# Optimization experiments

Measured on AMD Instinct MI355X. Metric: run time of the kernel, lower is better.

The kernel has to match this reference:

```python
import jax, jax.numpy as jnp
import numpy as np

N, E = 50000, 800000
DIM_IN, DIM_H, DIM_OUT, HEADS = 128, 16, 64, 8
NEG_SLOPE = 0.2  # PyG GATv2Conv default


def setup_inputs() -> dict:
    key = jax.random.key(0)
    ks = jax.random.split(key, 10)
    s = 0.1
    x = jax.random.normal(ks[0], (N, DIM_IN), jnp.float32)
    edge_index = jax.random.randint(ks[1], (2, E), 0, N, dtype=jnp.int32)
    Wl1 = jax.random.normal(ks[2], (DIM_IN, HEADS * DIM_H), jnp.float32) * s
    Wr1 = jax.random.normal(ks[3], (DIM_IN, HEADS * DIM_H), jnp.float32) * s
    att1 = jax.random.normal(ks[4], (HEADS, DIM_H), jnp.float32) * s
    b1 = jnp.zeros((HEADS * DIM_H,), jnp.float32)
    Wl2 = jax.random.normal(ks[5], (HEADS * DIM_H, DIM_OUT), jnp.float32) * s
    Wr2 = jax.random.normal(ks[6], (HEADS * DIM_H, DIM_OUT), jnp.float32) * s
    att2 = jax.random.normal(ks[7], (1, DIM_OUT), jnp.float32) * s
    b2 = jnp.zeros((DIM_OUT,), jnp.float32)
    return dict(x=x, edge_index=edge_index, Wl1=Wl1, Wr1=Wr1, att1=att1, b1=b1,
                Wl2=Wl2, Wr2=Wr2, att2=att2, b2=b2)


def gatv2_conv(x, src, dst, Wl, Wr, att, bias, heads, out_ch):
    # PyG GATv2Conv (share_weights=False, concat=True)
    n = x.shape[0]
    xl = (x @ Wl).reshape(n, heads, out_ch)  # source-side transform
    xr = (x @ Wr).reshape(n, heads, out_ch)  # target-side transform
    e = jax.nn.leaky_relu(xl[src] + xr[dst], NEG_SLOPE)          # [E, H, C]
    logits = jnp.einsum('ehc,hc->eh', e, att)                    # [E, H]
    # segment softmax over incoming edges of each dst node
    m = jax.lax.stop_gradient(jax.ops.segment_max(logits, dst, num_segments=n))
    ex = jnp.exp(logits - m[dst])
    denom = jax.ops.segment_sum(ex, dst, num_segments=n)
    alpha = ex / denom[dst]                                      # [E, H]
    out = jax.ops.segment_sum(xl[src] * alpha[..., None], dst, num_segments=n)
    return out.reshape(n, heads * out_ch) + bias


def reference(x, edge_index, Wl1, Wr1, att1, b1, Wl2, Wr2, att2, b2):
    n = x.shape[0]
    loops = jnp.arange(n, dtype=edge_index.dtype)
    src = jnp.concatenate([edge_index[0], loops])  # add_self_loops=True
    dst = jnp.concatenate([edge_index[1], loops])
    h = gatv2_conv(x, src, dst, Wl1, Wr1, att1, b1, HEADS, DIM_H)
    h = jax.nn.elu(h)
    out = gatv2_conv(h, src, dst, Wl2, Wr2, att2, b2, 1, DIM_OUT)
    return jax.nn.log_softmax(out, axis=1)
```

## Files before the change

### kernel.cpp

```cpp
#include <hip/hip_runtime.h>
#include <cstdint>

#define DIM_IN 128
#define HEADS 8
#define DIM_H 16
#define H1 128
#define DIM_OUT 64
#define NEG 0.2f
#define CAP 6144

typedef __attribute__((ext_vector_type(8))) short bf16x8;
typedef __attribute__((ext_vector_type(4))) float f32x4;

__device__ __forceinline__ float blo(uint32_t u) { return __uint_as_float(u << 16); }
__device__ __forceinline__ float bhi(uint32_t u) { return __uint_as_float(u & 0xffff0000u); }
__device__ __forceinline__ unsigned short f2b(float f) {
  uint32_t u = __float_as_uint(f);
  u += 0x7fffu + ((u >> 16) & 1u);
  return (unsigned short)(u >> 16);
}

__global__ __launch_bounds__(256) void conv_x(
    const float* __restrict__ in, unsigned short* __restrict__ out, int total) {
  int i = (blockIdx.x * 256 + threadIdx.x) * 8;
  if (i >= total) return;
  float4 a = *(const float4*)(in + i);
  float4 b = *(const float4*)(in + i + 4);
  ushort4 u0 = {f2b(a.x), f2b(a.y), f2b(a.z), f2b(a.w)};
  ushort4 u1 = {f2b(b.x), f2b(b.y), f2b(b.z), f2b(b.w)};
  *(ushort4*)(out + i) = u0;
  *(ushort4*)(out + i + 4) = u1;
}

__global__ __launch_bounds__(256) void prep_w(
    const float* __restrict__ W0, const float* __restrict__ W1,
    const float* __restrict__ W2, const float* __restrict__ W3,
    unsigned short* __restrict__ T0, unsigned short* __restrict__ T1,
    unsigned short* __restrict__ T2, unsigned short* __restrict__ T3) {
  int z = blockIdx.y;
  const float* W = (z == 0) ? W0 : (z == 1) ? W1 : (z == 2) ? W2 : W3;
  unsigned short* T = (z == 0) ? T0 : (z == 1) ? T1 : (z == 2) ? T2 : T3;
  int M = (z < 2) ? 128 : 64;
  int t = blockIdx.x * 256 + threadIdx.x;
  if (t >= M * 128) return;
  int n = t >> 7, k = t & 127;
  T[t] = f2b(W[k * M + n]);
}

template <int M>
__global__ __launch_bounds__(256) void gemm_mfma(
    const unsigned short* __restrict__ A,
    const unsigned short* __restrict__ Bt0, const unsigned short* __restrict__ Bt1,
    unsigned short* __restrict__ Cb0, float* __restrict__ C1, int Nrows) {
  constexpr int K = 128;
  constexpr int LDA = 72;
  constexpr int MT = M / 2;
  constexpr int NT = MT / 16;
  __shared__ __align__(16) short Asm[128 * LDA];
  __shared__ __align__(16) short Bsm[M * LDA];
  const unsigned short* __restrict__ Bt = blockIdx.z ? Bt1 : Bt0;
  const int row0 = blockIdx.x * 128;
  const int tid = threadIdx.x;
  const int w = tid >> 6, lane = tid & 63;
  const int l = lane & 15, q = lane >> 4;
  const int wrow = (w >> 1) * 64, wcol = (w & 1) * MT;

  f32x4 zero = {0.f, 0.f, 0.f, 0.f};
  f32x4 acc[4][NT];
#pragma unroll
  for (int ti = 0; ti < 4; ++ti)
#pragma unroll
    for (int tj = 0; tj < NT; ++tj) acc[ti][tj] = zero;

  for (int k0 = 0; k0 < K; k0 += 64) {
    __syncthreads();
    {
      int r = tid >> 1, sg = (tid & 1) * 32;
      int grow = row0 + r;
      const uint4* src = (const uint4*)(A + (size_t)grow * K + k0 + sg);
      uint4 z4 = make_uint4(0, 0, 0, 0);
#pragma unroll
      for (int i = 0; i < 4; ++i) {
        uint4 v = (grow < Nrows) ? src[i] : z4;
        *(uint4*)(Asm + r * LDA + sg + i * 8) = v;
      }
    }
    {
      int r = tid >> 1, sg = (tid & 1) * 32;
      if (r < M) {
        const uint4* src = (const uint4*)(Bt + (size_t)r * K + k0 + sg);
#pragma unroll
        for (int i = 0; i < 4; ++i)
          *(uint4*)(Bsm + r * LDA + sg + i * 8) = src[i];
      }
    }
    __syncthreads();
#pragma unroll
    for (int kk = 0; kk < 64; kk += 32) {
      bf16x8 af[4], bfr[NT];
#pragma unroll
      for (int ti = 0; ti < 4; ++ti)
        af[ti] = *(const bf16x8*)(Asm + (wrow + ti * 16 + l) * LDA + kk + q * 8);
#pragma unroll
      for (int tj = 0; tj < NT; ++tj)
        bfr[tj] = *(const bf16x8*)(Bsm + (wcol + tj * 16 + l) * LDA + kk + q * 8);
#pragma unroll
      for (int ti = 0; ti < 4; ++ti)
#pragma unroll
        for (int tj = 0; tj < NT; ++tj)
          acc[ti][tj] = __builtin_amdgcn_mfma_f32_16x16x32_bf16(
              af[ti], bfr[tj], acc[ti][tj], 0, 0, 0);
    }
  }
#pragma unroll
  for (int ti = 0; ti < 4; ++ti) {
#pragma unroll
    for (int tj = 0; tj < NT; ++tj) {
      int col = wcol + tj * 16 + l;
#pragma unroll
      for (int r = 0; r < 4; ++r) {
        int grow = row0 + wrow + ti * 16 + q * 4 + r;
        if (grow < Nrows) {
          float vv = acc[ti][tj][r];
          if (blockIdx.z == 0) Cb0[(size_t)grow * M + col] = f2b(vv);
          else                 C1[(size_t)grow * M + col] = vv;
        }
      }
    }
  }
}

__global__ __launch_bounds__(256) void p1_bucket(
    const int* __restrict__ ei, int* __restrict__ gcnt,
    uint32_t* __restrict__ gbuf, int E, int nbkt) {
  __shared__ int hist[256];
  __shared__ int base[256];
  __shared__ int cur[256];
  int tid = threadIdx.x;
  hist[tid] = 0;
  __syncthreads();
  int e0 = blockIdx.x * 8192;
  int nE = min(8192, E - e0);
  for (int i = tid; i < nE; i += 256)
    atomicAdd(&hist[ei[E + e0 + i] >> 8], 1);
  __syncthreads();
  if (tid < nbkt) {
    int h = hist[tid];
    base[tid] = h ? atomicAdd(&gcnt[tid], h) : 0;
  }
  cur[tid] = 0;
  __syncthreads();
  for (int i = tid; i < nE; i += 256) {
    int d = ei[E + e0 + i];
    int s = ei[e0 + i];
    int b = d >> 8;
    int r = atomicAdd(&cur[b], 1);
    int pos = base[b] + r;
    if (pos < CAP) gbuf[(size_t)b * CAP + pos] = ((uint32_t)d << 16) | (uint32_t)s;
  }
}

__device__ __forceinline__ int block_excl_scan256(int v, int* tmp) {
  int lane = threadIdx.x & 63, wid = threadIdx.x >> 6;
  int x = v;
#pragma unroll
  for (int o = 1; o < 64; o <<= 1) {
    int y = __shfl_up(x, o, 64);
    if (lane >= o) x += y;
  }
  if (lane == 63) tmp[wid] = x;
  __syncthreads();
  int prefix = 0;
#pragma unroll
  for (int w = 0; w < 4; ++w) if (w < wid) prefix += tmp[w];
  __syncthreads();
  return prefix + x - v;
}

__global__ __launch_bounds__(256) void p2_fused(
    const uint32_t* __restrict__ gbuf, const int* __restrict__ gcnt,
    int* __restrict__ off, int* __restrict__ srcs, int N, int nbkt) {
  __shared__ int sb[256];
  __shared__ int hist[256];
  __shared__ int cur[256];
  __shared__ int tmp[4];
  int b = blockIdx.x, tid = threadIdx.x;
  int gv = (tid < nbkt) ? gcnt[tid] : 0;
  int gex = block_excl_scan256(gv, tmp);
  sb[tid] = gex;
  hist[tid] = 0;
  __syncthreads();
  int base = sb[b];
  int cnt = min(gcnt[b], CAP);
  const uint32_t* p = gbuf + (size_t)b * CAP;
  for (int i = tid; i < cnt; i += 256)
    atomicAdd(&hist[(p[i] >> 16) & 255], 1);
  __syncthreads();
  int d = hist[tid];
  int excl = block_excl_scan256(d, tmp);
  int idx = (b << 8) + tid;
  int o = base + excl;
  if (idx <= N) off[idx] = o;
  cur[tid] = o;
  __syncthreads();
  for (int i = tid; i < cnt; i += 256) {
    uint32_t v = p[i];
    int pos = atomicAdd(&cur[(v >> 16) & 255], 1);
    srcs[pos] = (int)(v & 0xFFFFu);
  }
}

__global__ __launch_bounds__(256) void agg_l1(
    const int* __restrict__ srcs, const int* __restrict__ off,
    const unsigned short* __restrict__ xlb, const float* __restrict__ xr,
    const float* __restrict__ att, const float* __restrict__ b1,
    unsigned short* __restrict__ hbb, int N) {
  int wid = threadIdx.x >> 6, lane = threadIdx.x & 63;
  int node = blockIdx.x * 4 + wid;
  if (node >= N) return;
  const int l4 = lane & 15;
  const int g  = lane >> 4;
  float4 xr0 = *(const float4*)(xr + ((size_t)node << 7) + (l4 << 3));
  float4 xr1 = *(const float4*)(xr + ((size_t)node << 7) + (l4 << 3) + 4);
  float4 a0  = *(const float4*)(att + (l4 << 3));
  float4 a1  = *(const float4*)(att + (l4 << 3) + 4);
  float acc0 = 0.f, acc1 = 0.f, acc2 = 0.f, acc3 = 0.f;
  float acc4 = 0.f, acc5 = 0.f, acc6 = 0.f, acc7 = 0.f;
  float dsum = 0.f;
  int beg = off[node];
  int M = off[node + 1] - beg + 1;
  for (int base = 0; base < M; base += 64) {
    int nk = min(64, M - base);
    int v = base + lane;
    int sv = 0;
    if (lane < nk) sv = (v == 0) ? node : srcs[beg + v - 1];
    int niter = (nk + 3) >> 2;
    for (int it = 0; it < niter; ++it) {
      int j = (it << 2) + g;
      int s = __shfl(sv, j, 64);
      uint4 xu = *(const uint4*)(xlb + ((size_t)s << 7) + (l4 << 3));
      float x0 = blo(xu.x), x1 = bhi(xu.x), x2 = blo(xu.y), x3 = bhi(xu.y);
      float x4 = blo(xu.z), x5 = bhi(xu.z), x6 = blo(xu.w), x7 = bhi(xu.w);
      float t, p;
      t = x0 + xr0.x; t = t > 0.f ? t : NEG * t; p = a0.x * t;
      t = x1 + xr0.y; t = t > 0.f ? t : NEG * t; p = fmaf(a0.y, t, p);
      t = x2 + xr0.z; t = t > 0.f ? t : NEG * t; p = fmaf(a0.z, t, p);
      t = x3 + xr0.w; t = t > 0.f ? t : NEG * t; p = fmaf(a0.w, t, p);
      t = x4 + xr1.x; t = t > 0.f ? t : NEG * t; p = fmaf(a1.x, t, p);
      t = x5 + xr1.y; t = t > 0.f ? t : NEG * t; p = fmaf(a1.y, t, p);
      t = x6 + xr1.z; t = t > 0.f ? t : NEG * t; p = fmaf(a1.z, t, p);
      t = x7 + xr1.w; t = t > 0.f ? t : NEG * t; p = fmaf(a1.w, t, p);
      p += __shfl_xor(p, 1, 64);
      float ev = (j < nk) ? __expf(p) : 0.f;
      acc0 = fmaf(ev, x0, acc0); acc1 = fmaf(ev, x1, acc1);
      acc2 = fmaf(ev, x2, acc2); acc3 = fmaf(ev, x3, acc3);
      acc4 = fmaf(ev, x4, acc4); acc5 = fmaf(ev, x5, acc5);
      acc6 = fmaf(ev, x6, acc6); acc7 = fmaf(ev, x7, acc7);
      dsum += ev;
    }
  }
#pragma unroll
  for (int o = 16; o <= 32; o <<= 1) {
    dsum += __shfl_xor(dsum, o, 64);
    acc0 += __shfl_xor(acc0, o, 64); acc1 += __shfl_xor(acc1, o, 64);
    acc2 += __shfl_xor(acc2, o, 64); acc3 += __shfl_xor(acc3, o, 64);
    acc4 += __shfl_xor(acc4, o, 64); acc5 += __shfl_xor(acc5, o, 64);
    acc6 += __shfl_xor(acc6, o, 64); acc7 += __shfl_xor(acc7, o, 64);
  }
  if (g == 0) {
    float inv = 1.0f / dsum;
    float4 bv0 = *(const float4*)(b1 + (l4 << 3));
    float4 bv1 = *(const float4*)(b1 + (l4 << 3) + 4);
    float o0 = fmaf(acc0, inv, bv0.x), o1 = fmaf(acc1, inv, bv0.y);
    float o2 = fmaf(acc2, inv, bv0.z), o3 = fmaf(acc3, inv, bv0.w);
    float o4 = fmaf(acc4, inv, bv1.x), o5 = fmaf(acc5, inv, bv1.y);
    float o6 = fmaf(acc6, inv, bv1.z), o7 = fmaf(acc7, inv, bv1.w);
    o0 = o0 > 0.f ? o0 : expm1f(o0); o1 = o1 > 0.f ? o1 : expm1f(o1);
    o2 = o2 > 0.f ? o2 : expm1f(o2); o3 = o3 > 0.f ? o3 : expm1f(o3);
    o4 = o4 > 0.f ? o4 : expm1f(o4); o5 = o5 > 0.f ? o5 : expm1f(o5);
    o6 = o6 > 0.f ? o6 : expm1f(o6); o7 = o7 > 0.f ? o7 : expm1f(o7);
    ushort4 h0 = {f2b(o0), f2b(o1), f2b(o2), f2b(o3)};
    ushort4 h1 = {f2b(o4), f2b(o5), f2b(o6), f2b(o7)};
    unsigned short* ph = hbb + ((size_t)node << 7) + (l4 << 3);
    *(ushort4*)(ph)     = h0;
    *(ushort4*)(ph + 4) = h1;
  }
}

__global__ __launch_bounds__(256) void agg_l2(
    const int* __restrict__ srcs, const int* __restrict__ off,
    const unsigned short* __restrict__ xlb, const float* __restrict__ xr,
    const float* __restrict__ att, const float* __restrict__ b2,
    float* __restrict__ out, int N) {
  int wid = threadIdx.x >> 6, lane = threadIdx.x & 63;
  int node = blockIdx.x * 4 + wid;
  if (node >= N) return;
  const int l3 = lane & 7;
  const int g  = lane >> 3;
  float4 xr0 = *(const float4*)(xr + ((size_t)node << 6) + (l3 << 3));
  float4 xr1 = *(const float4*)(xr + ((size_t)node << 6) + (l3 << 3) + 4);
  float4 a0  = *(const float4*)(att + (l3 << 3));
  float4 a1  = *(const float4*)(att + (l3 << 3) + 4);
  float acc0 = 0.f, acc1 = 0.f, acc2 = 0.f, acc3 = 0.f;
  float acc4 = 0.f, acc5 = 0.f, acc6 = 0.f, acc7 = 0.f;
  float dsum = 0.f;
  int beg = off[node];
  int M = off[node + 1] - beg + 1;
  for (int base = 0; base < M; base += 64) {
    int nk = min(64, M - base);
    int v = base + lane;
    int sv = 0;
    if (lane < nk) sv = (v == 0) ? node : srcs[beg + v - 1];
    int niter = (nk + 7) >> 3;
    for (int it = 0; it < niter; ++it) {
      int j = (it << 3) + g;
      int s = __shfl(sv, j, 64);
      uint4 xu = *(const uint4*)(xlb + ((size_t)s << 6) + (l3 << 3));
      float x0 = blo(xu.x), x1 = bhi(xu.x), x2 = blo(xu.y), x3 = bhi(xu.y);
      float x4 = blo(xu.z), x5 = bhi(xu.z), x6 = blo(xu.w), x7 = bhi(xu.w);
      float t, p;
      t = x0 + xr0.x; t = t > 0.f ? t : NEG * t; p = a0.x * t;
      t = x1 + xr0.y; t = t > 0.f ? t : NEG * t; p = fmaf(a0.y, t, p);
      t = x2 + xr0.z; t = t > 0.f ? t : NEG * t; p = fmaf(a0.z, t, p);
      t = x3 + xr0.w; t = t > 0.f ? t : NEG * t; p = fmaf(a0.w, t, p);
      t = x4 + xr1.x; t = t > 0.f ? t : NEG * t; p = fmaf(a1.x, t, p);
      t = x5 + xr1.y; t = t > 0.f ? t : NEG * t; p = fmaf(a1.y, t, p);
      t = x6 + xr1.z; t = t > 0.f ? t : NEG * t; p = fmaf(a1.z, t, p);
      t = x7 + xr1.w; t = t > 0.f ? t : NEG * t; p = fmaf(a1.w, t, p);
      p += __shfl_xor(p, 1, 64);
      p += __shfl_xor(p, 2, 64);
      p += __shfl_xor(p, 4, 64);
      float ev = (j < nk) ? __expf(p) : 0.f;
      acc0 = fmaf(ev, x0, acc0); acc1 = fmaf(ev, x1, acc1);
      acc2 = fmaf(ev, x2, acc2); acc3 = fmaf(ev, x3, acc3);
      acc4 = fmaf(ev, x4, acc4); acc5 = fmaf(ev, x5, acc5);
      acc6 = fmaf(ev, x6, acc6); acc7 = fmaf(ev, x7, acc7);
      dsum += ev;
    }
  }
#pragma unroll
  for (int o = 8; o <= 32; o <<= 1) {
    dsum += __shfl_xor(dsum, o, 64);
    acc0 += __shfl_xor(acc0, o, 64); acc1 += __shfl_xor(acc1, o, 64);
    acc2 += __shfl_xor(acc2, o, 64); acc3 += __shfl_xor(acc3, o, 64);
    acc4 += __shfl_xor(acc4, o, 64); acc5 += __shfl_xor(acc5, o, 64);
    acc6 += __shfl_xor(acc6, o, 64); acc7 += __shfl_xor(acc7, o, 64);
  }
  float inv = 1.0f / dsum;
  float4 bv0 = *(const float4*)(b2 + (l3 << 3));
  float4 bv1 = *(const float4*)(b2 + (l3 << 3) + 4);
  float v0 = fmaf(acc0, inv, bv0.x), v1 = fmaf(acc1, inv, bv0.y);
  float v2 = fmaf(acc2, inv, bv0.z), v3 = fmaf(acc3, inv, bv0.w);
  float v4 = fmaf(acc4, inv, bv1.x), v5 = fmaf(acc5, inv, bv1.y);
  float v6 = fmaf(acc6, inv, bv1.z), v7 = fmaf(acc7, inv, bv1.w);
  float m = fmaxf(fmaxf(fmaxf(v0, v1), fmaxf(v2, v3)),
                  fmaxf(fmaxf(v4, v5), fmaxf(v6, v7)));
#pragma unroll
  for (int o = 1; o <= 4; o <<= 1) m = fmaxf(m, __shfl_xor(m, o, 64));
  float s = __expf(v0 - m) + __expf(v1 - m) + __expf(v2 - m) + __expf(v3 - m)
          + __expf(v4 - m) + __expf(v5 - m) + __expf(v6 - m) + __expf(v7 - m);
#pragma unroll
  for (int o = 1; o <= 4; o <<= 1) s += __shfl_xor(s, o, 64);
  if (g == 0) {
    float ls = __logf(s) + m;
    float* po = out + ((size_t)node << 6) + (l3 << 3);
    *(float4*)(po)     = make_float4(v0 - ls, v1 - ls, v2 - ls, v3 - ls);
    *(float4*)(po + 4) = make_float4(v4 - ls, v5 - ls, v6 - ls, v7 - ls);
  }
}

extern "C" void kernel_launch(void* const* d_in, const int* in_sizes, int n_in,
                              void* d_out, int out_size, void* d_ws, size_t ws_size,
                              hipStream_t stream) {
  const float* x    = (const float*)d_in[0];
  const int*   ei   = (const int*)d_in[1];
  const float* Wl1  = (const float*)d_in[2];
  const float* Wr1  = (const float*)d_in[3];
  const float* att1 = (const float*)d_in[4];
  const float* b1   = (const float*)d_in[5];
  const float* Wl2  = (const float*)d_in[6];
  const float* Wr2  = (const float*)d_in[7];
  const float* att2 = (const float*)d_in[8];
  const float* b2   = (const float*)d_in[9];
  float* out = (float*)d_out;

  const int N = in_sizes[0] / DIM_IN;
  const int E = in_sizes[1] / 2;
  const int nb = (N + 255) / 256;

  float* ws = (float*)d_ws;
  const size_t szNH = (size_t)N * H1;
  float* xr1 = ws;
  float* xr2 = ws + szNH;
  unsigned short* xb   = (unsigned short*)(ws + szNH + (size_t)N * DIM_OUT);
  unsigned short* xlb1 = xb + szNH;
  unsigned short* hbb  = xlb1 + szNH;
  unsigned short* xlb2 = hbb + szNH;
  unsigned short* wt0  = xlb2 + (size_t)N * DIM_OUT;
  unsigned short* wt1  = wt0 + 16384;
  unsigned short* wt2  = wt1 + 16384;
  unsigned short* wt3  = wt2 + 8192;
  int* ibase  = (int*)(wt3 + 8192);
  int* off    = ibase;
  int* gcnt   = ibase + N + 1;
  int* srcs   = ibase + N + 1 + 256;
  uint32_t* gbuf = (uint32_t*)(srcs + E);

  hipMemsetAsync(gcnt, 0, 256 * sizeof(int), stream);
  p1_bucket<<<(E + 8191) / 8192, 256, 0, stream>>>(ei, gcnt, gbuf, E, nb);
  p2_fused<<<nb, 256, 0, stream>>>(gbuf, gcnt, off, srcs, N, nb);

  int totx = N * DIM_IN;
  conv_x<<<(totx / 8 + 255) / 256, 256, 0, stream>>>(x, xb, totx);
  prep_w<<<dim3(64, 4), 256, 0, stream>>>(Wl1, Wr1, Wl2, Wr2, wt0, wt1, wt2, wt3);

  const int gb = (N + 127) / 128;

  gemm_mfma<128><<<dim3(gb, 1, 2), 256, 0, stream>>>(xb, wt0, wt1, xlb1, xr1, N);
  agg_l1<<<(N + 3) / 4, 256, 0, stream>>>(srcs, off, xlb1, xr1, att1, b1, hbb, N);

  gemm_mfma<64><<<dim3(gb, 1, 2), 256, 0, stream>>>(hbb, wt2, wt3, xlb2, xr2, N);
  agg_l2<<<(N + 3) / 4, 256, 0, stream>>>(srcs, off, xlb2, xr2, att2, b2, out, N);
}
```

Before: 255.2 us.

## Split leaky-ReLU logits into per-node linear terms plus abs term, use exp2

Rewrites leaky_relu(z) as 0.6z + 0.4|z|, so the linear part of each attention logit splits into a per-source term (precomputed by new dotp kernels) and a per-destination term (computed once per node), and only the abs term stays in the per-edge loop. Constants are pre-scaled by log2(e) so exp2f replaces __expf. The x-conversion and weight-prep kernels are fused into one launch. In exchange it adds two small kernels, an extra per-edge scalar gather of dL, and slight rounding differences from the regrouped arithmetic.

```diff
diff --git a/kernel.cpp b/kernel.cpp
--- a/kernel.cpp
+++ b/kernel.cpp
@@ -8,6 +8,7 @@
 #define DIM_OUT 64
 #define NEG 0.2f
 #define CAP 6144
+#define L2E 1.4426950408889634f
 
 typedef __attribute__((ext_vector_type(8))) short bf16x8;
 typedef __attribute__((ext_vector_type(4))) float f32x4;
@@ -20,31 +21,71 @@
   return (unsigned short)(u >> 16);
 }
 
-__global__ __launch_bounds__(256) void conv_x(
-    const float* __restrict__ in, unsigned short* __restrict__ out, int total) {
-  int i = (blockIdx.x * 256 + threadIdx.x) * 8;
-  if (i >= total) return;
-  float4 a = *(const float4*)(in + i);
-  float4 b = *(const float4*)(in + i + 4);
-  ushort4 u0 = {f2b(a.x), f2b(a.y), f2b(a.z), f2b(a.w)};
-  ushort4 u1 = {f2b(b.x), f2b(b.y), f2b(b.z), f2b(b.w)};
-  *(ushort4*)(out + i) = u0;
-  *(ushort4*)(out + i + 4) = u1;
-}
-
-__global__ __launch_bounds__(256) void prep_w(
+__global__ __launch_bounds__(256) void prep_fused(
+    const float* __restrict__ x, unsigned short* __restrict__ xb, int totx,
     const float* __restrict__ W0, const float* __restrict__ W1,
     const float* __restrict__ W2, const float* __restrict__ W3,
     unsigned short* __restrict__ T0, unsigned short* __restrict__ T1,
-    unsigned short* __restrict__ T2, unsigned short* __restrict__ T3) {
-  int z = blockIdx.y;
-  const float* W = (z == 0) ? W0 : (z == 1) ? W1 : (z == 2) ? W2 : W3;
-  unsigned short* T = (z == 0) ? T0 : (z == 1) ? T1 : (z == 2) ? T2 : T3;
-  int M = (z < 2) ? 128 : 64;
+    unsigned short* __restrict__ T2, unsigned short* __restrict__ T3,
+    int xblocks) {
+  int bx = blockIdx.x;
+  if (bx < xblocks) {
+    int i = (bx * 256 + threadIdx.x) * 8;
+    if (i >= totx) return;
+    float4 a = *(const float4*)(x + i);
+    float4 b = *(const float4*)(x + i + 4);
+    ushort4 u0 = {f2b(a.x), f2b(a.y), f2b(a.z), f2b(a.w)};
+    ushort4 u1 = {f2b(b.x), f2b(b.y), f2b(b.z), f2b(b.w)};
+    *(ushort4*)(xb + i) = u0;
+    *(ushort4*)(xb + i + 4) = u1;
+  } else {
+    int wz = bx - xblocks;
+    int z = wz >> 6;
+    const float* W = (z == 0) ? W0 : (z == 1) ? W1 : (z == 2) ? W2 : W3;
+    unsigned short* T = (z == 0) ? T0 : (z == 1) ? T1 : (z == 2) ? T2 : T3;
+    int M = (z < 2) ? 128 : 64;
+    int t = (wz & 63) * 256 + threadIdx.x;
+    if (t >= M * 128) return;
+    int n = t >> 7, k = t & 127;
+    T[t] = f2b(W[k * M + n]);
+  }
+}
+
+__global__ __launch_bounds__(256) void dotp1(
+    const unsigned short* __restrict__ xlb, const float* __restrict__ att,
+    float* __restrict__ dL, int N8) {
   int t = blockIdx.x * 256 + threadIdx.x;
-  if (t >= M * 128) return;
-  int n = t >> 7, k = t & 127;
-  T[t] = f2b(W[k * M + n]);
+  if (t >= N8) return;
+  int h = t & 7;
+  const uint4* p = (const uint4*)(xlb + ((size_t)t << 4));
+  uint4 u0 = p[0], u1 = p[1];
+  const float4* pa = (const float4*)(att + (h << 4));
+  float4 a0 = pa[0], a1 = pa[1], a2 = pa[2], a3 = pa[3];
+  float s = a0.x * blo(u0.x) + a0.y * bhi(u0.x) + a0.z * blo(u0.y) + a0.w * bhi(u0.y)
+          + a1.x * blo(u0.z) + a1.y * bhi(u0.z) + a1.z * blo(u0.w) + a1.w * bhi(u0.w)
+          + a2.x * blo(u1.x) + a2.y * bhi(u1.x) + a2.z * blo(u1.y) + a2.w * bhi(u1.y)
+          + a3.x * blo(u1.z) + a3.y * bhi(u1.z) + a3.z * blo(u1.w) + a3.w * bhi(u1.w);
+  dL[t] = s * (0.6f * L2E);
+}
+
+__global__ __launch_bounds__(256) void dotp2(
+    const unsigned short* __restrict__ xlb, const float* __restrict__ att,
+    float* __restrict__ dL, int N) {
+  int t = blockIdx.x * 256 + threadIdx.x;
+  int n = t >> 1, half = t & 1;
+  if (n >= N) return;
+  const uint4* p = (const uint4*)(xlb + ((size_t)n << 6) + (half << 5));
+  const float4* pa = (const float4*)(att + (half << 5));
+  float s = 0.f;
+#pragma unroll
+  for (int i = 0; i < 4; ++i) {
+    uint4 u = p[i];
+    float4 aa = pa[2 * i], ab = pa[2 * i + 1];
+    s += aa.x * blo(u.x) + aa.y * bhi(u.x) + aa.z * blo(u.y) + aa.w * bhi(u.y)
+       + ab.x * blo(u.z) + ab.y * bhi(u.z) + ab.z * blo(u.w) + ab.w * bhi(u.w);
+  }
+  s += __shfl_xor(s, 1, 64);
+  if (half == 0) dL[n] = s * (0.6f * L2E);
 }
 
 template <int M>
@@ -214,16 +255,24 @@
     const int* __restrict__ srcs, const int* __restrict__ off,
     const unsigned short* __restrict__ xlb, const float* __restrict__ xr,
     const float* __restrict__ att, const float* __restrict__ b1,
-    unsigned short* __restrict__ hbb, int N) {
+    const float* __restrict__ dL, unsigned short* __restrict__ hbb, int N) {
   int wid = threadIdx.x >> 6, lane = threadIdx.x & 63;
   int node = blockIdx.x * 4 + wid;
   if (node >= N) return;
   const int l4 = lane & 15;
   const int g  = lane >> 4;
+  const int hh = l4 >> 1;
   float4 xr0 = *(const float4*)(xr + ((size_t)node << 7) + (l4 << 3));
   float4 xr1 = *(const float4*)(xr + ((size_t)node << 7) + (l4 << 3) + 4);
   float4 a0  = *(const float4*)(att + (l4 << 3));
   float4 a1  = *(const float4*)(att + (l4 << 3) + 4);
+  const float K04 = 0.4f * L2E;
+  float c40 = K04 * a0.x, c41 = K04 * a0.y, c42 = K04 * a0.z, c43 = K04 * a0.w;
+  float c44 = K04 * a1.x, c45 = K04 * a1.y, c46 = K04 * a1.z, c47 = K04 * a1.w;
+  float dr = a0.x * xr0.x + a0.y * xr0.y + a0.z * xr0.z + a0.w * xr0.w
+           + a1.x * xr1.x + a1.y * xr1.y + a1.z * xr1.z + a1.w * xr1.w;
+  dr += __shfl_xor(dr, 1, 64);
+  dr *= 0.6f * L2E;
   float acc0 = 0.f, acc1 = 0.f, acc2 = 0.f, acc3 = 0.f;
   float acc4 = 0.f, acc5 = 0.f, acc6 = 0.f, acc7 = 0.f;
   float dsum = 0.f;
@@ -239,19 +288,22 @@
       int j = (it << 2) + g;
       int s = __shfl(sv, j, 64);
       uint4 xu = *(const uint4*)(xlb + ((size_t)s << 7) + (l4 << 3));
+      float dl = dL[(s << 3) + hh];
       float x0 = blo(xu.x), x1 = bhi(xu.x), x2 = blo(xu.y), x3 = bhi(xu.y);
       float x4 = blo(xu.z), x5 = bhi(xu.z), x6 = blo(xu.w), x7 = bhi(xu.w);
-      float t, p;
-      t = x0 + xr0.x; t = t > 0.f ? t : NEG * t; p = a0.x * t;
-      t = x1 + xr0.y; t = t > 0.f ? t : NEG * t; p = fmaf(a0.y, t, p);
-      t = x2 + xr0.z; t = t > 0.f ? t : NEG * t; p = fmaf(a0.z, t, p);
-      t = x3 + xr0.w; t = t > 0.f ? t : NEG * t; p = fmaf(a0.w, t, p);
-      t = x4 + xr1.x; t = t > 0.f ? t : NEG * t; p = fmaf(a1.x, t, p);
-      t = x5 + xr1.y; t = t > 0.f ? t : NEG * t; p = fmaf(a1.y, t, p);
-      t = x6 + xr1.z; t = t > 0.f ? t : NEG * t; p = fmaf(a1.z, t, p);
-      t = x7 + xr1.w; t = t > 0.f ? t : NEG * t; p = fmaf(a1.w, t, p);
+      float z, pA, pB;
+      z = x0 + xr0.x; pA = c40 * fabsf(z);
+      z = x1 + xr0.y; pA = fmaf(c41, fabsf(z), pA);
+      z = x2 + xr0.z; pA = fmaf(c42, fabsf(z), pA);
+      z = x3 + xr0.w; pA = fmaf(c43, fabsf(z), pA);
+      z = x4 + xr1.x; pB = c44 * fabsf(z);
+      z = x5 + xr1.y; pB = fmaf(c45, fabsf(z), pB);
+      z = x6 + xr1.z; pB = fmaf(c46, fabsf(z), pB);
+      z = x7 + xr1.w; pB = fmaf(c47, fabsf(z), pB);
+      float p = pA + pB;
       p += __shfl_xor(p, 1, 64);
-      float ev = (j < nk) ? __expf(p) : 0.f;
+      p += dl + dr;
+      float ev = (j < nk) ? exp2f(p) : 0.f;
       acc0 = fmaf(ev, x0, acc0); acc1 = fmaf(ev, x1, acc1);
       acc2 = fmaf(ev, x2, acc2); acc3 = fmaf(ev, x3, acc3);
       acc4 = fmaf(ev, x4, acc4); acc5 = fmaf(ev, x5, acc5);
@@ -291,7 +343,7 @@
     const int* __restrict__ srcs, const int* __restrict__ off,
     const unsigned short* __restrict__ xlb, const float* __restrict__ xr,
     const float* __restrict__ att, const float* __restrict__ b2,
-    float* __restrict__ out, int N) {
+    const float* __restrict__ dL, float* __restrict__ out, int N) {
   int wid = threadIdx.x >> 6, lane = threadIdx.x & 63;
   int node = blockIdx.x * 4 + wid;
   if (node >= N) return;
@@ -301,6 +353,15 @@
   float4 xr1 = *(const float4*)(xr + ((size_t)node << 6) + (l3 << 3) + 4);
   float4 a0  = *(const float4*)(att + (l3 << 3));
   float4 a1  = *(const float4*)(att + (l3 << 3) + 4);
+  const float K04 = 0.4f * L2E;
+  float c40 = K04 * a0.x, c41 = K04 * a0.y, c42 = K04 * a0.z, c43 = K04 * a0.w;
+  float c44 = K04 * a1.x, c45 = K04 * a1.y, c46 = K04 * a1.z, c47 = K04 * a1.w;
+  float dr = a0.x * xr0.x + a0.y * xr0.y + a0.z * xr0.z + a0.w * xr0.w
+           + a1.x * xr1.x + a1.y * xr1.y + a1.z * xr1.z + a1.w * xr1.w;
+  dr += __shfl_xor(dr, 1, 64);
+  dr += __shfl_xor(dr, 2, 64);
+  dr += __shfl_xor(dr, 4, 64);
+  dr *= 0.6f * L2E;
   float acc0 = 0.f, acc1 = 0.f, acc2 = 0.f, acc3 = 0.f;
   float acc4 = 0.f, acc5 = 0.f, acc6 = 0.f, acc7 = 0.f;
   float dsum = 0.f;
@@ -316,21 +377,24 @@
       int j = (it << 3) + g;
       int s = __shfl(sv, j, 64);
       uint4 xu = *(const uint4*)(xlb + ((size_t)s << 6) + (l3 << 3));
+      float dl = dL[s];
       float x0 = blo(xu.x), x1 = bhi(xu.x), x2 = blo(xu.y), x3 = bhi(xu.y);
       float x4 = blo(xu.z), x5 = bhi(xu.z), x6 = blo(xu.w), x7 = bhi(xu.w);
-      float t, p;
-      t = x0 + xr0.x; t = t > 0.f ? t : NEG * t; p = a0.x * t;
-      t = x1 + xr0.y; t = t > 0.f ? t : NEG * t; p = fmaf(a0.y, t, p);
-      t = x2 + xr0.z; t = t > 0.f ? t : NEG * t; p = fmaf(a0.z, t, p);
-      t = x3 + xr0.w; t = t > 0.f ? t : NEG * t; p = fmaf(a0.w, t, p);
-      t = x4 + xr1.x; t = t > 0.f ? t : NEG * t; p = fmaf(a1.x, t, p);
-      t = x5 + xr1.y; t = t > 0.f ? t : NEG * t; p = fmaf(a1.y, t, p);
-      t = x6 + xr1.z; t = t > 0.f ? t : NEG * t; p = fmaf(a1.z, t, p);
-      t = x7 + xr1.w; t = t > 0.f ? t : NEG * t; p = fmaf(a1.w, t, p);
+      float z, pA, pB;
+      z = x0 + xr0.x; pA = c40 * fabsf(z);
+      z = x1 + xr0.y; pA = fmaf(c41, fabsf(z), pA);
+      z = x2 + xr0.z; pA = fmaf(c42, fabsf(z), pA);
+      z = x3 + xr0.w; pA = fmaf(c43, fabsf(z), pA);
+      z = x4 + xr1.x; pB = c44 * fabsf(z);
+      z = x5 + xr1.y; pB = fmaf(c45, fabsf(z), pB);
+      z = x6 + xr1.z; pB = fmaf(c46, fabsf(z), pB);
+      z = x7 + xr1.w; pB = fmaf(c47, fabsf(z), pB);
+      float p = pA + pB;
       p += __shfl_xor(p, 1, 64);
       p += __shfl_xor(p, 2, 64);
       p += __shfl_xor(p, 4, 64);
-      float ev = (j < nk) ? __expf(p) : 0.f;
+      p += dl + dr;
+      float ev = (j < nk) ? exp2f(p) : 0.f;
       acc0 = fmaf(ev, x0, acc0); acc1 = fmaf(ev, x1, acc1);
       acc2 = fmaf(ev, x2, acc2); acc3 = fmaf(ev, x3, acc3);
       acc4 = fmaf(ev, x4, acc4); acc5 = fmaf(ev, x5, acc5);
@@ -392,7 +456,9 @@
   const size_t szNH = (size_t)N * H1;
   float* xr1 = ws;
   float* xr2 = ws + szNH;
-  unsigned short* xb   = (unsigned short*)(ws + szNH + (size_t)N * DIM_OUT);
+  float* dL1 = ws + szNH + (size_t)N * DIM_OUT;
+  float* dL2 = dL1 + (size_t)N * 8;
+  unsigned short* xb   = (unsigned short*)(dL2 + N);
   unsigned short* xlb1 = xb + szNH;
   unsigned short* hbb  = xlb1 + szNH;
   unsigned short* xlb2 = hbb + szNH;
@@ -411,14 +477,17 @@
   p2_fused<<<nb, 256, 0, stream>>>(gbuf, gcnt, off, srcs, N, nb);
 
   int totx = N * DIM_IN;
-  conv_x<<<(totx / 8 + 255) / 256, 256, 0, stream>>>(x, xb, totx);
-  prep_w<<<dim3(64, 4), 256, 0, stream>>>(Wl1, Wr1, Wl2, Wr2, wt0, wt1, wt2, wt3);
+  int xblocks = (totx / 8 + 255) / 256;
+  prep_fused<<<xblocks + 256, 256, 0, stream>>>(
+      x, xb, totx, Wl1, Wr1, Wl2, Wr2, wt0, wt1, wt2, wt3, xblocks);
 
   const int gb = (N + 127) / 128;
 
   gemm_mfma<128><<<dim3(gb, 1, 2), 256, 0, stream>>>(xb, wt0, wt1, xlb1, xr1, N);
-  agg_l1<<<(N + 3) / 4, 256, 0, stream>>>(srcs, off, xlb1, xr1, att1, b1, hbb, N);
+  dotp1<<<(N * 8 + 255) / 256, 256, 0, stream>>>(xlb1, att1, dL1, N * 8);
+  agg_l1<<<(N + 3) / 4, 256, 0, stream>>>(srcs, off, xlb1, xr1, att1, b1, dL1, hbb, N);
 
   gemm_mfma<64><<<dim3(gb, 1, 2), 256, 0, stream>>>(hbb, wt2, wt3, xlb2, xr2, N);
-  agg_l2<<<(N + 3) / 4, 256, 0, stream>>>(srcs, off, xlb2, xr2, att2, b2, out, N);
-}
+  dotp2<<<(N * 2 + 255) / 256, 256, 0, stream>>>(xlb2, att2, dL2, N);
+  agg_l2<<<(N + 3) / 4, 256, 0, stream>>>(srcs, off, xlb2, xr2, att2, b2, dL2, out, N);
+}
```

New measurement: 273.1 us. 7.0% more time.
